# Kernel tuning notes

Measured on AMD Instinct MI355X. Metric: run time of the kernel, lower is better.

Reference implementation:

```python
import jax, jax.numpy as jnp
import numpy as np

SR = 16000
FRAME_LENGTH = 2048
HOP = 512
WIN_LENGTH = 30
FREQ_LOW = 85
FREQ_HIGH = 3400
EPS = 1e-9


def setup_inputs() -> dict:
    key = jax.random.key(0)
    waveform = jax.random.normal(key, (8, 960000), dtype=jnp.float32)
    return {"waveform": waveform}


def _detect_pitch(w):
    # w: [B, T] padded waveform. Mirrors torchaudio.functional.detect_pitch_frequency.
    B, T = w.shape
    frame_size = int(np.ceil(SR * (HOP / SR)))          # = HOP = 512
    lags = int(np.ceil(SR / FREQ_LOW))                  # 189
    num_frames = int(np.ceil(T / frame_size))
    p = lags + num_frames * frame_size - T
    wp = jnp.pad(w, ((0, 0), (0, p)))                   # [B, lags + F*fs]
    frames = wp[:, : num_frames * frame_size].reshape(B, num_frames, frame_size)
    s1n = (EPS + jnp.linalg.norm(frames, axis=-1)) ** 2  # [B, F], lag-independent

    def body(carry, lag):
        seg = jax.lax.dynamic_slice_in_dim(wp, lag, num_frames * frame_size, axis=1)
        seg = seg.reshape(B, num_frames, frame_size)
        num = jnp.sum(frames * seg, axis=-1)
        s2n = (EPS + jnp.linalg.norm(seg, axis=-1)) ** 2
        return carry, num / s1n / s2n

    _, nccf = jax.lax.scan(body, None, jnp.arange(1, lags + 1))  # [lags, B, F]
    nccf = jnp.moveaxis(nccf, 0, -1)                             # [B, F, lags]

    # _find_max_per_frame
    lag_min = int(np.ceil(SR / FREQ_HIGH))  # 5
    half_size = lags // 2                   # 94
    best_v = jnp.max(nccf[..., lag_min:], axis=-1)
    best_i = jnp.argmax(nccf[..., lag_min:], axis=-1)
    half_v = jnp.max(nccf[..., lag_min:half_size], axis=-1)
    half_i = jnp.argmax(nccf[..., lag_min:half_size], axis=-1)
    mask = half_v > 0.99 * best_v           # prefer near-max with smallest lag
    idx = jnp.where(mask, half_i, best_i) + lag_min + 1  # +1 calibration offset

    # lower median (sorted index (n-1)//2). Output length = F - (WIN_LENGTH-1-pad_len).
    pad_len = (WIN_LENGTH - 1) // 2         # 14
    padded = jnp.concatenate([jnp.tile(idx[:, :1], (1, pad_len)), idx], axis=-1)
    out_len = padded.shape[-1] - WIN_LENGTH + 1
    win_idx = jnp.arange(out_len)[:, None] + jnp.arange(WIN_LENGTH)[None, :]
    wins = padded[:, win_idx]               # [B, out_len, WIN_LENGTH]
    med = jnp.sort(wins, axis=-1)[..., (WIN_LENGTH - 1) // 2]

    return SR / (EPS + med.astype(jnp.float32))


def reference(waveform):
    pad = FRAME_LENGTH // 2
    wpad = jnp.pad(waveform, ((0, 0), (pad, pad)), mode="reflect")
    pitch = _detect_pitch(wpad)
    desired = waveform.shape[-1] // HOP + 1
    if pitch.shape[-1] > desired:
        pitch = pitch[..., :desired]
    else:
        pitch = jnp.pad(pitch, ((0, 0), (0, desired - pitch.shape[-1])))
    return pitch
```

## Files before the change

### kernel.cpp

```cpp
#include <hip/hip_runtime.h>

#define T_WPAD  962048
#define T_RAW   960000
#define NFRM    1879
#define OUTW    1876
#define MEDLEN  1864
#define WINL    30
#define PADL    14
#define FPB     16
#define NBX     118
#define XLEN    8392
#define X4LEN   2098

__global__ __launch_bounds__(256) void nccf_kernel(const float* __restrict__ wav,
                                                   int* __restrict__ idxArr) {
    const int bx   = blockIdx.x;
    const int b    = blockIdx.y;
    const int tid  = threadIdx.x;
    const int wave = tid >> 6;
    const int lane = tid & 63;
    const int g    = lane >> 4;
    const int s    = lane & 15;

    __shared__ __align__(16) float X[XLEN];
    __shared__ float Pw1[FPB][190];
    __shared__ float Pw2[FPB][190];

    const long a0 = (long)bx * (FPB * 512);
    const float* wrow = wav + (long)b * T_RAW;

    if (bx >= 1 && bx <= NBX - 2) {
        const float4* src = (const float4*)(wrow + (a0 - 1024));
        float4* dst = (float4*)X;
        for (int i = tid; i < X4LEN; i += 256) dst[i] = src[i];
    } else {
        for (int i = tid; i < XLEN; i += 256) {
            float v = 0.0f;
            long t = a0 + i;
            if (t < T_WPAD) {
                long u = t - 1024;
                if (u < 0) u = -u;
                if (u >= T_RAW) u = 2L * (T_RAW - 1) - u;
                v = wrow[u];
            }
            X[i] = v;
        }
    }
    __syncthreads();

    const int F  = wave * 4 + g;
    const int gf = bx * FPB + F;
    const bool valid = (gf < NFRM);
    const float* Xf = X + F * 512;

    {
        const float* p = Xf + s * 44;
        double run = 0.0;
        #pragma unroll
        for (int m = 0; m < 44; ++m) { double x = (double)p[m]; run = fma(x, x, run); }
        double inc = run;
        #pragma unroll
        for (int off = 1; off < 16; off <<= 1) {
            double v = __shfl_up(inc, off, 16);
            if (s >= off) inc += v;
        }
        double run2 = inc - run;
        #pragma unroll
        for (int m = 0; m < 44; ++m) {
            double x = (double)p[m];
            run2 = fma(x, x, run2);
            int idx = s * 44 + m + 1;
            float val = (float)run2;
            if (idx <= 189)                     Pw1[F][idx - 1]   = val;
            else if (idx >= 512 && idx <= 701)  Pw2[F][idx - 512] = val;
        }
    }

    float acc[12];
    #pragma unroll
    for (int r = 0; r < 12; ++r) acc[r] = 0.0f;
    {
        const float4* X4 = (const float4*)X;
        const int aBase = F * 128;
        const int wBase = aBase + 3 * s;
        float w[16];
        #pragma unroll
        for (int d = 0; d < 4; ++d) {
            float4 t4 = X4[wBase + d];
            w[4 * d] = t4.x; w[4 * d + 1] = t4.y; w[4 * d + 2] = t4.z; w[4 * d + 3] = t4.w;
        }
        float4 A = X4[aBase];
        #pragma unroll 4
        for (int k = 0; k < 127; ++k) {
            float4 An = X4[aBase + k + 1];
            float4 nx = X4[wBase + k + 4];
            #pragma unroll
            for (int r = 0; r < 12; ++r) {
                acc[r] = fmaf(A.x, w[r + 1], acc[r]);
                acc[r] = fmaf(A.y, w[r + 2], acc[r]);
                acc[r] = fmaf(A.z, w[r + 3], acc[r]);
                acc[r] = fmaf(A.w, w[r + 4], acc[r]);
            }
            #pragma unroll
            for (int i = 0; i < 12; ++i) w[i] = w[i + 4];
            w[12] = nx.x; w[13] = nx.y; w[14] = nx.z; w[15] = nx.w;
            A = An;
        }
        #pragma unroll
        for (int r = 0; r < 12; ++r) {
            acc[r] = fmaf(A.x, w[r + 1], acc[r]);
            acc[r] = fmaf(A.y, w[r + 2], acc[r]);
            acc[r] = fmaf(A.z, w[r + 3], acc[r]);
            acc[r] = fmaf(A.w, w[r + 4], acc[r]);
        }
    }

    float bestv = -1e30f, halfv = -1e30f;
    int bestk = 1 << 30, halfk = 1 << 30;
    {
        float s1 = 1e-9f + sqrtf(Pw2[F][0]);
        float s1n = s1 * s1;
        #pragma unroll
        for (int r = 1; r <= 12; ++r) {
            int lag  = 12 * s + r;
            int kidx = lag - 1;
            if (kidx <= 188) {
                float q  = Pw2[F][lag] - Pw1[F][lag - 1];
                float s2 = 1e-9f + sqrtf(q);
                float v  = acc[r - 1] / s1n / (s2 * s2);
                if (kidx >= 5) {
                    if (v > bestv) { bestv = v; bestk = kidx; }
                    if (kidx <= 93 && v > halfv) { halfv = v; halfk = kidx; }
                }
            }
        }
    }

    #pragma unroll
    for (int off = 8; off >= 1; off >>= 1) {
        float ov = __shfl_xor(bestv, off, 16); int ok = __shfl_xor(bestk, off, 16);
        if (ov > bestv || (ov == bestv && ok < bestk)) { bestv = ov; bestk = ok; }
        float hv = __shfl_xor(halfv, off, 16); int hk = __shfl_xor(halfk, off, 16);
        if (hv > halfv || (hv == halfv && hk < halfk)) { halfv = hv; halfk = hk; }
    }

    if (valid && s == 0) {
        bool m = (halfv > 0.99f * bestv);
        int sel = m ? halfk : bestk;
        idxArr[b * NFRM + gf] = sel + 1;
    }
}

__global__ __launch_bounds__(256) void med_kernel(const int* __restrict__ idxArr,
                                                  float* __restrict__ out) {
    int gid = blockIdx.x * 256 + threadIdx.x;
    if (gid >= 8 * OUTW) return;
    int b = gid / OUTW;
    int i = gid - b * OUTW;
    float o = 0.0f;
    if (i < MEDLEN) {
        const int* row = idxArr + b * NFRM;
        int vals[WINL];
        #pragma unroll
        for (int m = 0; m < WINL; ++m) {
            int sIdx = i + m - PADL;
            vals[m] = row[sIdx < 0 ? 0 : sIdx];
        }
        int med = vals[0];
        #pragma unroll
        for (int c = 0; c < WINL; ++c) {
            int cl = 0, ce = 0;
            #pragma unroll
            for (int m = 0; m < WINL; ++m) {
                cl += (vals[m] <  vals[c]) ? 1 : 0;
                ce += (vals[m] == vals[c]) ? 1 : 0;
            }
            if (cl <= 14 && 14 < cl + ce) med = vals[c];
        }
        o = 16000.0f / (1e-9f + (float)med);
    }
    out[gid] = o;
}

extern "C" void kernel_launch(void* const* d_in, const int* in_sizes, int n_in,
                              void* d_out, int out_size, void* d_ws, size_t ws_size,
                              hipStream_t stream) {
    const float* wav = (const float*)d_in[0];
    float* out = (float*)d_out;
    int* idxArr = (int*)d_ws;

    dim3 gB(NBX, 8);
    hipLaunchKernelGGL(nccf_kernel, gB, dim3(256), 0, stream, wav, idxArr);

    int total = 8 * OUTW;
    hipLaunchKernelGGL(med_kernel, dim3((total + 255) / 256), dim3(256), 0, stream,
                       idxArr, out);
}
```

Baseline: 72.00 us.

## Compute segment energies in-register during correlation loop, drop shared prefix sums

The separate double-precision prefix-sum pass and the Pw1/Pw2 shared-memory tables are replaced. Each lane now accumulates the sliding-window energy from the samples it already streams through the correlation loop, and derives its 12 per-lag energies from register values. The frame energy is broadcast from lane 0 by a shuffle. This removes a pass over shared memory, the shuffle scan and about 12 KB of shared memory, which may allow more blocks per CU. In exchange the main loop gains double-precision adds and more registers, and is split into two segments.

```diff
diff --git a/kernel.cpp b/kernel.cpp
--- a/kernel.cpp
+++ b/kernel.cpp
@@ -23,8 +23,6 @@
     const int s    = lane & 15;
 
     __shared__ __align__(16) float X[XLEN];
-    __shared__ float Pw1[FPB][190];
-    __shared__ float Pw2[FPB][190];
 
     const long a0 = (long)bx * (FPB * 512);
     const float* wrow = wav + (long)b * T_RAW;
@@ -51,47 +49,32 @@
     const int F  = wave * 4 + g;
     const int gf = bx * FPB + F;
     const bool valid = (gf < NFRM);
-    const float* Xf = X + F * 512;
-
-    {
-        const float* p = Xf + s * 44;
-        double run = 0.0;
-        #pragma unroll
-        for (int m = 0; m < 44; ++m) { double x = (double)p[m]; run = fma(x, x, run); }
-        double inc = run;
-        #pragma unroll
-        for (int off = 1; off < 16; off <<= 1) {
-            double v = __shfl_up(inc, off, 16);
-            if (s >= off) inc += v;
-        }
-        double run2 = inc - run;
-        #pragma unroll
-        for (int m = 0; m < 44; ++m) {
-            double x = (double)p[m];
-            run2 = fma(x, x, run2);
-            int idx = s * 44 + m + 1;
-            float val = (float)run2;
-            if (idx <= 189)                     Pw1[F][idx - 1]   = val;
-            else if (idx >= 512 && idx <= 701)  Pw2[F][idx - 512] = val;
-        }
-    }
 
     float acc[12];
     #pragma unroll
     for (int r = 0; r < 12; ++r) acc[r] = 0.0f;
+    float sq[12];
+    double Tcur = 0.0;
+    double T512 = 0.0;
+    float w[16];
+
     {
         const float4* X4 = (const float4*)X;
         const int aBase = F * 128;
         const int wBase = aBase + 3 * s;
-        float w[16];
         #pragma unroll
         for (int d = 0; d < 4; ++d) {
             float4 t4 = X4[wBase + d];
             w[4 * d] = t4.x; w[4 * d + 1] = t4.y; w[4 * d + 2] = t4.z; w[4 * d + 3] = t4.w;
         }
+        #pragma unroll
+        for (int j = 0; j < 12; ++j) sq[j] = w[j] * w[j];
+        #pragma unroll
+        for (int j = 0; j < 16; ++j) Tcur += (double)(w[j] * w[j]);
+
         float4 A = X4[aBase];
         #pragma unroll 4
-        for (int k = 0; k < 127; ++k) {
+        for (int k = 0; k < 124; ++k) {
             float4 An = X4[aBase + k + 1];
             float4 nx = X4[wBase + k + 4];
             #pragma unroll
@@ -101,6 +84,25 @@
                 acc[r] = fmaf(A.z, w[r + 3], acc[r]);
                 acc[r] = fmaf(A.w, w[r + 4], acc[r]);
             }
+            float quad = fmaf(nx.x, nx.x, fmaf(nx.y, nx.y, fmaf(nx.z, nx.z, nx.w * nx.w)));
+            Tcur += (double)quad;
+            #pragma unroll
+            for (int i = 0; i < 12; ++i) w[i] = w[i + 4];
+            w[12] = nx.x; w[13] = nx.y; w[14] = nx.z; w[15] = nx.w;
+            A = An;
+        }
+        T512 = Tcur;
+        #pragma unroll
+        for (int k = 124; k < 127; ++k) {
+            float4 An = X4[aBase + k + 1];
+            float4 nx = X4[wBase + k + 4];
+            #pragma unroll
+            for (int r = 0; r < 12; ++r) {
+                acc[r] = fmaf(A.x, w[r + 1], acc[r]);
+                acc[r] = fmaf(A.y, w[r + 2], acc[r]);
+                acc[r] = fmaf(A.z, w[r + 3], acc[r]);
+                acc[r] = fmaf(A.w, w[r + 4], acc[r]);
+            }
             #pragma unroll
             for (int i = 0; i < 12; ++i) w[i] = w[i + 4];
             w[12] = nx.x; w[13] = nx.y; w[14] = nx.z; w[15] = nx.w;
@@ -115,18 +117,30 @@
         }
     }
 
+    double qv[12];
+    {
+        double Thi = T512, Tlo = 0.0;
+        #pragma unroll
+        for (int r = 1; r <= 12; ++r) {
+            float eh = w[3 + r];
+            Thi += (double)(eh * eh);
+            Tlo += (double)sq[r - 1];
+            qv[r - 1] = Thi - Tlo;
+        }
+    }
+    double s1d = __shfl(T512, 0, 16);
+
     float bestv = -1e30f, halfv = -1e30f;
     int bestk = 1 << 30, halfk = 1 << 30;
     {
-        float s1 = 1e-9f + sqrtf(Pw2[F][0]);
+        float s1 = 1e-9f + sqrtf((float)s1d);
         float s1n = s1 * s1;
         #pragma unroll
         for (int r = 1; r <= 12; ++r) {
             int lag  = 12 * s + r;
             int kidx = lag - 1;
             if (kidx <= 188) {
-                float q  = Pw2[F][lag] - Pw1[F][lag - 1];
-                float s2 = 1e-9f + sqrtf(q);
+                float s2 = 1e-9f + sqrtf((float)qv[r - 1]);
                 float v  = acc[r - 1] / s1n / (s2 * s2);
                 if (kidx >= 5) {
                     if (v > bestv) { bestv = v; bestk = kidx; }
```

Measured after the change: 66.76 us. 1.08x faster.
